# Optimization experiments

Hardware: AMD Instinct MI355X
Metric: run time of the kernel (lower is better)

Reference implementation:

```python
import jax, jax.numpy as jnp
import numpy as np

B, IN, H, NOPT = 16384, 4096, 128, 64
GAIN = 0.5  # default control_gains value in the module


def gru_cell(x, h, Wih, Whh, bih, bhh):
    # torch GRU single step; gate order r, z, n
    gi = x @ Wih + bih          # [B, 3H]
    gh = h @ Whh + bhh          # [B, 3H]
    ir, iz, inn = jnp.split(gi, 3, axis=-1)
    hr, hz, hn = jnp.split(gh, 3, axis=-1)
    r = jax.nn.sigmoid(ir + hr)
    z = jax.nn.sigmoid(iz + hz)
    n = jnp.tanh(inn + r * hn)
    return (1.0 - z) * n + z * h


def setup_inputs() -> dict:
    key = jax.random.key(0)
    ks = jax.random.split(key, 12)
    s = lambda k, shape: (jax.random.normal(k, shape, jnp.float32) * 0.05)
    return {
        "obs": jax.random.normal(ks[0], (B, IN), jnp.float32),
        "chosen_option": jax.random.randint(ks[1], (B,), 0, NOPT),
        "h0": jnp.zeros((B, H), jnp.float32),
        "h1": jnp.zeros((B, H), jnp.float32),
        "Wa": s(ks[2], (IN, H)), "ba": jnp.zeros((H,), jnp.float32),
        "Wih0": s(ks[3], (H, 3 * H)), "Whh0": s(ks[4], (H, 3 * H)),
        "bih0": jnp.zeros((3 * H,), jnp.float32), "bhh0": jnp.zeros((3 * H,), jnp.float32),
        "Wih1": s(ks[5], (2 * H, 3 * H)), "Whh1": s(ks[6], (H, 3 * H)),
        "bih1": jnp.zeros((3 * H,), jnp.float32), "bhh1": jnp.zeros((3 * H,), jnp.float32),
        "Wv0": s(ks[7], (H, NOPT)), "bv0": jnp.zeros((NOPT,), jnp.float32),
        "Wv1": s(ks[8], (H, NOPT)), "bv1": jnp.zeros((NOPT,), jnp.float32),
        "Wt0": s(ks[9], (H, NOPT)), "bt0": jnp.zeros((NOPT,), jnp.float32),
    }


def reference(obs, chosen_option, h0, h1, Wa, ba, Wih0, Whh0, bih0, bhh0,
              Wih1, Whh1, bih1, bhh1, Wv0, bv0, Wv1, bv1, Wt0, bt0):
    # attention: tanh(Linear(obs))
    attn = jnp.tanh(obs @ Wa + ba)                       # [B, H]
    # layer 0: GRU on attn
    h0n = gru_cell(attn, h0, Wih0, Whh0, bih0, bhh0)     # [B, H]
    hc0 = (h0n - 0.5) * GAIN + 0.5                       # gain contrast
    v0 = hc0 @ Wv0 + bv0                                 # [B, NOPT]
    term = jax.nn.sigmoid(hc0 @ Wt0 + bt0)               # [B, NOPT]
    term_p = jnp.take_along_axis(term, chosen_option[:, None], axis=1)  # [B, 1]
    # layer 1: GRU on cat(attn, own hidden)
    x1 = jnp.concatenate([attn, h1], axis=-1)            # [B, 2H]
    h1n = gru_cell(x1, h1, Wih1, Whh1, bih1, bhh1)       # [B, H]
    hc1 = (h1n - 0.5) * GAIN + 0.5
    v1 = hc1 @ Wv1 + bv1                                 # [B, NOPT]
    return v0, term_p, v1, h0n, h1n
```

## Files before the change

kernel.cpp:

```cpp
#include <hip/hip_runtime.h>
#include <stdint.h>


typedef __attribute__((ext_vector_type(8))) short bf16x8;
typedef __attribute__((ext_vector_type(4))) float f32x4;
typedef __attribute__((ext_vector_type(8))) float f32x8;

#define INDIM 4096
#define H 128
#define NOPT 64

#define WS_WAT    0u
#define WS_WIH0T  524288u
#define WS_WHH0T  573440u
#define WS_WIH1T  622592u
#define WS_WHH1T  720896u
#define WS_WV0T   770048u
#define WS_WV1T   778240u
#define WS_WT0T   786432u

#define OUT_V0    0u
#define OUT_TERMP 1048576u
#define OUT_V1    1064960u
#define OUT_H0N   2113536u
#define OUT_H1N   4210688u

static __device__ __forceinline__ uint16_t f2bf(float f) {
  union { float f; uint32_t i; } x; x.f = f;
  uint32_t r = x.i + 0x7fffu + ((x.i >> 16) & 1u);
  return (uint16_t)(r >> 16);
}
static __device__ __forceinline__ float sigm(float x) { return 1.0f / (1.0f + __expf(-x)); }
static __device__ __forceinline__ float fast_tanh(float x) {
  float e = __expf(2.0f * x);
  return 1.0f - 2.0f / (e + 1.0f);
}
static __device__ __forceinline__ f32x4 mfma16(bf16x8 a, bf16x8 b, f32x4 c) {
  return __builtin_amdgcn_mfma_f32_16x16x32_bf16(a, b, c, 0, 0, 0);
}
static __device__ __forceinline__ bf16x8 cvt8(f32x8 v) {
  bf16x8 r;
#pragma unroll
  for (int j = 0; j < 8; ++j) r[j] = (short)f2bf(v[j]);
  return r;
}

__global__ void k_transpose(const float* __restrict__ Wa,
                            const float* __restrict__ Wih0,
                            const float* __restrict__ Whh0,
                            const float* __restrict__ Wih1,
                            const float* __restrict__ Whh1,
                            const float* __restrict__ Wv0,
                            const float* __restrict__ Wv1,
                            const float* __restrict__ Wt0,
                            uint16_t* __restrict__ ws) {
  int blk = blockIdx.x;
  const float* in; uint16_t* out; int ksh; int N; int base;
  if (blk < 2048)      { in = Wa;   out = ws + WS_WAT;   ksh = 12; N = 128; base = 0; }
  else if (blk < 2240) { in = Wih0; out = ws + WS_WIH0T; ksh = 7;  N = 384; base = 2048; }
  else if (blk < 2432) { in = Whh0; out = ws + WS_WHH0T; ksh = 7;  N = 384; base = 2240; }
  else if (blk < 2816) { in = Wih1; out = ws + WS_WIH1T; ksh = 8;  N = 384; base = 2432; }
  else if (blk < 3008) { in = Whh1; out = ws + WS_WHH1T; ksh = 7;  N = 384; base = 2816; }
  else if (blk < 3040) { in = Wv0;  out = ws + WS_WV0T;  ksh = 7;  N = 64;  base = 3008; }
  else if (blk < 3072) { in = Wv1;  out = ws + WS_WV1T;  ksh = 7;  N = 64;  base = 3040; }
  else                 { in = Wt0;  out = ws + WS_WT0T;  ksh = 7;  N = 64;  base = 3072; }
  int e = (blk - base) * 256 + (int)threadIdx.x;
  int n = e >> ksh;
  int k = e & ((1 << ksh) - 1);
  out[e] = f2bf(in[(size_t)k * N + n]);
}

__launch_bounds__(128)
__global__ void k_fused(const float* __restrict__ obs,
                        const uint16_t* __restrict__ ws,
                        const float* __restrict__ ba,
                        const float* __restrict__ h0,
                        const float* __restrict__ bih0,
                        const float* __restrict__ bhh0,
                        const float* __restrict__ bv0,
                        const float* __restrict__ bt0,
                        const int* __restrict__ chosen,
                        const float* __restrict__ h1,
                        const float* __restrict__ bih1,
                        const float* __restrict__ bhh1,
                        const float* __restrict__ bv1,
                        float* __restrict__ out) {
  __shared__ uint16_t sAttn[2][16 * 16 * 8];
  __shared__ uint16_t sHC[2][16 * 16 * 8];
  const uint16_t* WaT   = ws + WS_WAT;
  const uint16_t* Wih0T = ws + WS_WIH0T;
  const uint16_t* Whh0T = ws + WS_WHH0T;
  const uint16_t* Wih1T = ws + WS_WIH1T;
  const uint16_t* Whh1T = ws + WS_WHH1T;
  const uint16_t* Wv0T  = ws + WS_WV0T;
  const uint16_t* Wv1T  = ws + WS_WV1T;
  const uint16_t* Wt0T  = ws + WS_WT0T;
  const int t = threadIdx.x, w = t >> 6, lane = t & 63;
  const int l15 = lane & 15, quad = lane >> 4;
  const int row0 = blockIdx.x * 32 + w * 16;
  uint16_t* sX = sAttn[w];
  uint16_t* sC = sHC[w];

  f32x4 acc[8] = {};
  {
    const float* arow = obs + (size_t)(row0 + l15) * INDIM + quad * 8;
    const uint16_t* brow = WaT + (size_t)l15 * INDIM + quad * 8;
#pragma unroll 2
    for (int kt = 0; kt < 64; ++kt) {
      const int k0 = kt * 64;
      f32x8 av0 = *(const f32x8*)(arow + k0);
      f32x8 av1 = *(const f32x8*)(arow + k0 + 32);
      bf16x8 a0 = cvt8(av0);
      bf16x8 a1 = cvt8(av1);
#pragma unroll
      for (int nb = 0; nb < 8; ++nb) {
        const uint16_t* bp = brow + (size_t)(nb * 16) * INDIM + k0;
        bf16x8 b0 = *(const bf16x8*)(bp);
        bf16x8 b1 = *(const bf16x8*)(bp + 32);
        acc[nb] = mfma16(a0, b0, acc[nb]);
        acc[nb] = mfma16(a1, b1, acc[nb]);
      }
    }
  }
#pragma unroll
  for (int nb = 0; nb < 8; ++nb) {
    const int col = nb * 16 + l15;
    const float bav = ba[col];
    const int kb = col >> 3;
#pragma unroll
    for (int i = 0; i < 4; ++i) {
      const int r = quad * 4 + i;
      sX[(r * 16 + (kb ^ r)) * 8 + (col & 7)] = f2bf(fast_tanh(acc[nb][i] + bav));
    }
  }

  bf16x8 ax[4], ah[4];
  {
    const float* hrow = h0 + (size_t)(row0 + l15) * H + quad * 8;
#pragma unroll
    for (int ks = 0; ks < 4; ++ks) {
      const int kb = ks * 4 + quad;
      ax[ks] = *(const bf16x8*)&sX[(l15 * 16 + (kb ^ l15)) * 8];
      ah[ks] = cvt8(*(const f32x8*)(hrow + ks * 32));
    }
  }
#pragma unroll
  for (int nb = 0; nb < 8; ++nb) {
    f32x4 air = {}, ahr = {}, aiz = {}, ahz = {}, ain = {}, ahn = {};
    const int nrow = nb * 16 + l15;
#pragma unroll
    for (int ks = 0; ks < 4; ++ks) {
      const int k = ks * 32 + quad * 8;
      bf16x8 b;
      b = *(const bf16x8*)(Wih0T + (size_t)(nrow      ) * H + k); air = mfma16(ax[ks], b, air);
      b = *(const bf16x8*)(Wih0T + (size_t)(nrow + 128) * H + k); aiz = mfma16(ax[ks], b, aiz);
      b = *(const bf16x8*)(Wih0T + (size_t)(nrow + 256) * H + k); ain = mfma16(ax[ks], b, ain);
      b = *(const bf16x8*)(Whh0T + (size_t)(nrow      ) * H + k); ahr = mfma16(ah[ks], b, ahr);
      b = *(const bf16x8*)(Whh0T + (size_t)(nrow + 128) * H + k); ahz = mfma16(ah[ks], b, ahz);
      b = *(const bf16x8*)(Whh0T + (size_t)(nrow + 256) * H + k); ahn = mfma16(ah[ks], b, ahn);
    }
    const int col = nrow;
    const float b_ir = bih0[col],       b_hr = bhh0[col];
    const float b_iz = bih0[col + 128], b_hz = bhh0[col + 128];
    const float b_in = bih0[col + 256], b_hn = bhh0[col + 256];
    const int kb = col >> 3;
#pragma unroll
    for (int i = 0; i < 4; ++i) {
      const int r = quad * 4 + i;
      const int grow = row0 + r;
      const float rr = sigm(air[i] + ahr[i] + b_ir + b_hr);
      const float zz = sigm(aiz[i] + ahz[i] + b_iz + b_hz);
      const float nn = fast_tanh(ain[i] + b_in + rr * (ahn[i] + b_hn));
      const float hv = h0[(size_t)grow * H + col];
      const float hnew = (1.0f - zz) * nn + zz * hv;
      out[OUT_H0N + (size_t)grow * H + col] = hnew;
      sC[(r * 16 + (kb ^ r)) * 8 + (col & 7)] = f2bf(0.5f * hnew + 0.25f);
    }
  }
  {
    int ch[4];
#pragma unroll
    for (int i = 0; i < 4; ++i) ch[i] = chosen[row0 + quad * 4 + i];
    bf16x8 ac[4];
#pragma unroll
    for (int ks = 0; ks < 4; ++ks) {
      const int kb = ks * 4 + quad;
      ac[ks] = *(const bf16x8*)&sC[(l15 * 16 + (kb ^ l15)) * 8];
    }
#pragma unroll
    for (int vb = 0; vb < 4; ++vb) {
      f32x4 av = {}, at = {};
      const int nrow = vb * 16 + l15;
#pragma unroll
      for (int ks = 0; ks < 4; ++ks) {
        const int k = ks * 32 + quad * 8;
        bf16x8 b;
        b = *(const bf16x8*)(Wv0T + (size_t)nrow * H + k); av = mfma16(ac[ks], b, av);
        b = *(const bf16x8*)(Wt0T + (size_t)nrow * H + k); at = mfma16(ac[ks], b, at);
      }
      const int col = vb * 16 + l15;
      const float bvv = bv0[col], btv = bt0[col];
#pragma unroll
      for (int i = 0; i < 4; ++i) {
        const int grow = row0 + quad * 4 + i;
        out[OUT_V0 + (size_t)grow * NOPT + col] = av[i] + bvv;
        if (ch[i] == col)
          out[OUT_TERMP + grow] = sigm(at[i] + btv);
      }
    }
  }

  bf16x8 ah1[4];
  {
    const float* hrow = h1 + (size_t)(row0 + l15) * H + quad * 8;
#pragma unroll
    for (int ks = 0; ks < 4; ++ks)
      ah1[ks] = cvt8(*(const f32x8*)(hrow + ks * 32));
  }
#pragma unroll
  for (int nb = 0; nb < 8; ++nb) {
    f32x4 air = {}, ahr = {}, aiz = {}, ahz = {}, ain = {}, ahn = {};
    const int nrow = nb * 16 + l15;
#pragma unroll
    for (int ks = 0; ks < 8; ++ks) {
      const int k = ks * 32 + quad * 8;
      const bf16x8 a = (ks < 4) ? ax[ks] : ah1[ks - 4];
      bf16x8 b;
      b = *(const bf16x8*)(Wih1T + (size_t)(nrow      ) * 256 + k); air = mfma16(a, b, air);
      b = *(const bf16x8*)(Wih1T + (size_t)(nrow + 128) * 256 + k); aiz = mfma16(a, b, aiz);
      b = *(const bf16x8*)(Wih1T + (size_t)(nrow + 256) * 256 + k); ain = mfma16(a, b, ain);
    }
#pragma unroll
    for (int ks = 0; ks < 4; ++ks) {
      const int k = ks * 32 + quad * 8;
      bf16x8 b;
      b = *(const bf16x8*)(Whh1T + (size_t)(nrow      ) * H + k); ahr = mfma16(ah1[ks], b, ahr);
      b = *(const bf16x8*)(Whh1T + (size_t)(nrow + 128) * H + k); ahz = mfma16(ah1[ks], b, ahz);
      b = *(const bf16x8*)(Whh1T + (size_t)(nrow + 256) * H + k); ahn = mfma16(ah1[ks], b, ahn);
    }
    const int col = nrow;
    const float b_ir = bih1[col],       b_hr = bhh1[col];
    const float b_iz = bih1[col + 128], b_hz = bhh1[col + 128];
    const float b_in = bih1[col + 256], b_hn = bhh1[col + 256];
    const int kb = col >> 3;
#pragma unroll
    for (int i = 0; i < 4; ++i) {
      const int r = quad * 4 + i;
      const int grow = row0 + r;
      const float rr = sigm(air[i] + ahr[i] + b_ir + b_hr);
      const float zz = sigm(aiz[i] + ahz[i] + b_iz + b_hz);
      const float nn = fast_tanh(ain[i] + b_in + rr * (ahn[i] + b_hn));
      const float hv = h1[(size_t)grow * H + col];
      const float hnew = (1.0f - zz) * nn + zz * hv;
      out[OUT_H1N + (size_t)grow * H + col] = hnew;
      sC[(r * 16 + (kb ^ r)) * 8 + (col & 7)] = f2bf(0.5f * hnew + 0.25f);
    }
  }
  {
    bf16x8 ac[4];
#pragma unroll
    for (int ks = 0; ks < 4; ++ks) {
      const int kb = ks * 4 + quad;
      ac[ks] = *(const bf16x8*)&sC[(l15 * 16 + (kb ^ l15)) * 8];
    }
#pragma unroll
    for (int vb = 0; vb < 4; ++vb) {
      f32x4 av = {};
      const int nrow = vb * 16 + l15;
#pragma unroll
      for (int ks = 0; ks < 4; ++ks) {
        const int k = ks * 32 + quad * 8;
        bf16x8 b = *(const bf16x8*)(Wv1T + (size_t)nrow * H + k);
        av = mfma16(ac[ks], b, av);
      }
      const int col = vb * 16 + l15;
      const float bvv = bv1[col];
#pragma unroll
      for (int i = 0; i < 4; ++i) {
        const int grow = row0 + quad * 4 + i;
        out[OUT_V1 + (size_t)grow * NOPT + col] = av[i] + bvv;
      }
    }
  }
}

extern "C" void kernel_launch(void* const* d_in, const int* in_sizes, int n_in,
                              void* d_out, int out_size, void* d_ws, size_t ws_size,
                              hipStream_t stream) {
  (void)in_sizes; (void)n_in; (void)out_size; (void)ws_size;
  const float* obs    = (const float*)d_in[0];
  const int*   chosen = (const int*)d_in[1];
  const float* h0     = (const float*)d_in[2];
  const float* h1     = (const float*)d_in[3];
  const float* Wa     = (const float*)d_in[4];
  const float* ba     = (const float*)d_in[5];
  const float* Wih0   = (const float*)d_in[6];
  const float* Whh0   = (const float*)d_in[7];
  const float* bih0   = (const float*)d_in[8];
  const float* bhh0   = (const float*)d_in[9];
  const float* Wih1   = (const float*)d_in[10];
  const float* Whh1   = (const float*)d_in[11];
  const float* bih1   = (const float*)d_in[12];
  const float* bhh1   = (const float*)d_in[13];
  const float* Wv0    = (const float*)d_in[14];
  const float* bv0    = (const float*)d_in[15];
  const float* Wv1    = (const float*)d_in[16];
  const float* bv1    = (const float*)d_in[17];
  const float* Wt0    = (const float*)d_in[18];
  const float* bt0    = (const float*)d_in[19];
  uint16_t* ws  = (uint16_t*)d_ws;
  float*    out = (float*)d_out;

  hipLaunchKernelGGL(k_transpose, dim3(3104), dim3(256), 0, stream,
                     Wa, Wih0, Whh0, Wih1, Whh1, Wv0, Wv1, Wt0, ws);
  hipLaunchKernelGGL(k_fused, dim3(512), dim3(128), 0, stream,
                     obs, ws, ba, h0, bih0, bhh0, bv0, bt0, chosen,
                     h1, bih1, bhh1, bv1, out);
}
```

Baseline: 539.3 us.

## Split GRU columns across four waves per 16-row block to raise occupancy

Each block now handles 16 batch rows with 4 waves, and each wave computes 32 of the 128 hidden columns. The attention GEMM, both GRU cells and the value heads are partitioned the same way, with shared-memory tiles and __syncthreads between stages. The grid grows from 512×128 to 1024×256 threads, so many more waves are in flight to hide load latency on the large obs stream. The cost is that every wave re-reads and re-converts the same obs rows, relying on cache hits, and the kernel now needs block-wide barriers. The float-to-bf16 conversion also switches to the HIP intrinsic, which may map to a hardware instruction.

```diff
diff --git a/kernel.cpp b/kernel.cpp
--- a/kernel.cpp
+++ b/kernel.cpp
@@ -1,4 +1,5 @@
 #include <hip/hip_runtime.h>
+#include <hip/hip_bf16.h>
 #include <stdint.h>
 
 
@@ -26,9 +27,8 @@
 #define OUT_H1N   4210688u
 
 static __device__ __forceinline__ uint16_t f2bf(float f) {
-  union { float f; uint32_t i; } x; x.f = f;
-  uint32_t r = x.i + 0x7fffu + ((x.i >> 16) & 1u);
-  return (uint16_t)(r >> 16);
+  __hip_bfloat16 h = __float2bfloat16(f);
+  return __builtin_bit_cast(uint16_t, h);
 }
 static __device__ __forceinline__ float sigm(float x) { return 1.0f / (1.0f + __expf(-x)); }
 static __device__ __forceinline__ float fast_tanh(float x) {
@@ -70,7 +70,7 @@
   out[e] = f2bf(in[(size_t)k * N + n]);
 }
 
-__launch_bounds__(128)
+__launch_bounds__(256, 4)
 __global__ void k_fused(const float* __restrict__ obs,
                         const uint16_t* __restrict__ ws,
                         const float* __restrict__ ba,
@@ -85,8 +85,8 @@
                         const float* __restrict__ bhh1,
                         const float* __restrict__ bv1,
                         float* __restrict__ out) {
-  __shared__ uint16_t sAttn[2][16 * 16 * 8];
-  __shared__ uint16_t sHC[2][16 * 16 * 8];
+  __shared__ uint16_t sX[16 * 16 * 8];
+  __shared__ uint16_t sC[16 * 16 * 8];
   const uint16_t* WaT   = ws + WS_WAT;
   const uint16_t* Wih0T = ws + WS_WIH0T;
   const uint16_t* Whh0T = ws + WS_WHH0T;
@@ -97,42 +97,44 @@
   const uint16_t* Wt0T  = ws + WS_WT0T;
   const int t = threadIdx.x, w = t >> 6, lane = t & 63;
   const int l15 = lane & 15, quad = lane >> 4;
-  const int row0 = blockIdx.x * 32 + w * 16;
-  uint16_t* sX = sAttn[w];
-  uint16_t* sC = sHC[w];
-
-  f32x4 acc[8] = {};
-  {
-    const float* arow = obs + (size_t)(row0 + l15) * INDIM + quad * 8;
-    const uint16_t* brow = WaT + (size_t)l15 * INDIM + quad * 8;
+  const int row0 = blockIdx.x * 16;
+  const int nbA = 2 * w;
+
+  f32x4 acc0 = {}, acc1 = {};
+  {
+    const float*    arow  = obs + (size_t)(row0 + l15) * INDIM + quad * 8;
+    const uint16_t* brow0 = WaT + (size_t)(nbA * 16 + l15) * INDIM + quad * 8;
+    const uint16_t* brow1 = brow0 + (size_t)16 * INDIM;
 #pragma unroll 2
     for (int kt = 0; kt < 64; ++kt) {
       const int k0 = kt * 64;
       f32x8 av0 = *(const f32x8*)(arow + k0);
       f32x8 av1 = *(const f32x8*)(arow + k0 + 32);
+      bf16x8 b00 = *(const bf16x8*)(brow0 + k0);
+      bf16x8 b01 = *(const bf16x8*)(brow0 + k0 + 32);
+      bf16x8 b10 = *(const bf16x8*)(brow1 + k0);
+      bf16x8 b11 = *(const bf16x8*)(brow1 + k0 + 32);
       bf16x8 a0 = cvt8(av0);
       bf16x8 a1 = cvt8(av1);
-#pragma unroll
-      for (int nb = 0; nb < 8; ++nb) {
-        const uint16_t* bp = brow + (size_t)(nb * 16) * INDIM + k0;
-        bf16x8 b0 = *(const bf16x8*)(bp);
-        bf16x8 b1 = *(const bf16x8*)(bp + 32);
-        acc[nb] = mfma16(a0, b0, acc[nb]);
-        acc[nb] = mfma16(a1, b1, acc[nb]);
-      }
-    }
-  }
-#pragma unroll
-  for (int nb = 0; nb < 8; ++nb) {
-    const int col = nb * 16 + l15;
+      acc0 = mfma16(a0, b00, acc0);
+      acc0 = mfma16(a1, b01, acc0);
+      acc1 = mfma16(a0, b10, acc1);
+      acc1 = mfma16(a1, b11, acc1);
+    }
+  }
+#pragma unroll
+  for (int nbl = 0; nbl < 2; ++nbl) {
+    const f32x4 A = nbl ? acc1 : acc0;
+    const int col = (nbA + nbl) * 16 + l15;
     const float bav = ba[col];
     const int kb = col >> 3;
 #pragma unroll
     for (int i = 0; i < 4; ++i) {
       const int r = quad * 4 + i;
-      sX[(r * 16 + (kb ^ r)) * 8 + (col & 7)] = f2bf(fast_tanh(acc[nb][i] + bav));
-    }
-  }
+      sX[(r * 16 + (kb ^ r)) * 8 + (col & 7)] = f2bf(fast_tanh(A[i] + bav));
+    }
+  }
+  __syncthreads();
 
   bf16x8 ax[4], ah[4];
   {
@@ -145,9 +147,9 @@
     }
   }
 #pragma unroll
-  for (int nb = 0; nb < 8; ++nb) {
+  for (int nbl = 0; nbl < 2; ++nbl) {
+    const int nrow = (nbA + nbl) * 16 + l15;
     f32x4 air = {}, ahr = {}, aiz = {}, ahz = {}, ain = {}, ahn = {};
-    const int nrow = nb * 16 + l15;
 #pragma unroll
     for (int ks = 0; ks < 4; ++ks) {
       const int k = ks * 32 + quad * 8;
@@ -177,6 +179,8 @@
       sC[(r * 16 + (kb ^ r)) * 8 + (col & 7)] = f2bf(0.5f * hnew + 0.25f);
     }
   }
+  __syncthreads();
+
   {
     int ch[4];
 #pragma unroll
@@ -187,28 +191,26 @@
       const int kb = ks * 4 + quad;
       ac[ks] = *(const bf16x8*)&sC[(l15 * 16 + (kb ^ l15)) * 8];
     }
-#pragma unroll
-    for (int vb = 0; vb < 4; ++vb) {
-      f32x4 av = {}, at = {};
-      const int nrow = vb * 16 + l15;
-#pragma unroll
-      for (int ks = 0; ks < 4; ++ks) {
-        const int k = ks * 32 + quad * 8;
-        bf16x8 b;
-        b = *(const bf16x8*)(Wv0T + (size_t)nrow * H + k); av = mfma16(ac[ks], b, av);
-        b = *(const bf16x8*)(Wt0T + (size_t)nrow * H + k); at = mfma16(ac[ks], b, at);
-      }
-      const int col = vb * 16 + l15;
-      const float bvv = bv0[col], btv = bt0[col];
-#pragma unroll
-      for (int i = 0; i < 4; ++i) {
-        const int grow = row0 + quad * 4 + i;
-        out[OUT_V0 + (size_t)grow * NOPT + col] = av[i] + bvv;
-        if (ch[i] == col)
-          out[OUT_TERMP + grow] = sigm(at[i] + btv);
-      }
-    }
-  }
+    f32x4 av = {}, at = {};
+    const int nrow = w * 16 + l15;
+#pragma unroll
+    for (int ks = 0; ks < 4; ++ks) {
+      const int k = ks * 32 + quad * 8;
+      bf16x8 b;
+      b = *(const bf16x8*)(Wv0T + (size_t)nrow * H + k); av = mfma16(ac[ks], b, av);
+      b = *(const bf16x8*)(Wt0T + (size_t)nrow * H + k); at = mfma16(ac[ks], b, at);
+    }
+    const int col = nrow;
+    const float bvv = bv0[col], btv = bt0[col];
+#pragma unroll
+    for (int i = 0; i < 4; ++i) {
+      const int grow = row0 + quad * 4 + i;
+      out[OUT_V0 + (size_t)grow * NOPT + col] = av[i] + bvv;
+      if (ch[i] == col)
+        out[OUT_TERMP + grow] = sigm(at[i] + btv);
+    }
+  }
+  __syncthreads();
 
   bf16x8 ah1[4];
   {
@@ -218,9 +220,9 @@
       ah1[ks] = cvt8(*(const f32x8*)(hrow + ks * 32));
   }
 #pragma unroll
-  for (int nb = 0; nb < 8; ++nb) {
+  for (int nbl = 0; nbl < 2; ++nbl) {
+    const int nrow = (nbA + nbl) * 16 + l15;
     f32x4 air = {}, ahr = {}, aiz = {}, ahz = {}, ain = {}, ahn = {};
-    const int nrow = nb * 16 + l15;
 #pragma unroll
     for (int ks = 0; ks < 8; ++ks) {
       const int k = ks * 32 + quad * 8;
@@ -256,6 +258,8 @@
       sC[(r * 16 + (kb ^ r)) * 8 + (col & 7)] = f2bf(0.5f * hnew + 0.25f);
     }
   }
+  __syncthreads();
+
   {
     bf16x8 ac[4];
 #pragma unroll
@@ -263,23 +267,20 @@
       const int kb = ks * 4 + quad;
       ac[ks] = *(const bf16x8*)&sC[(l15 * 16 + (kb ^ l15)) * 8];
     }
-#pragma unroll
-    for (int vb = 0; vb < 4; ++vb) {
-      f32x4 av = {};
-      const int nrow = vb * 16 + l15;
-#pragma unroll
-      for (int ks = 0; ks < 4; ++ks) {
-        const int k = ks * 32 + quad * 8;
-        bf16x8 b = *(const bf16x8*)(Wv1T + (size_t)nrow * H + k);
-        av = mfma16(ac[ks], b, av);
-      }
-      const int col = vb * 16 + l15;
-      const float bvv = bv1[col];
-#pragma unroll
-      for (int i = 0; i < 4; ++i) {
-        const int grow = row0 + quad * 4 + i;
-        out[OUT_V1 + (size_t)grow * NOPT + col] = av[i] + bvv;
-      }
+    f32x4 av = {};
+    const int nrow = w * 16 + l15;
+#pragma unroll
+    for (int ks = 0; ks < 4; ++ks) {
+      const int k = ks * 32 + quad * 8;
+      bf16x8 b = *(const bf16x8*)(Wv1T + (size_t)nrow * H + k);
+      av = mfma16(ac[ks], b, av);
+    }
+    const int col = nrow;
+    const float bvv = bv1[col];
+#pragma unroll
+    for (int i = 0; i < 4; ++i) {
+      const int grow = row0 + quad * 4 + i;
+      out[OUT_V1 + (size_t)grow * NOPT + col] = av[i] + bvv;
     }
   }
 }
@@ -313,7 +314,7 @@
 
   hipLaunchKernelGGL(k_transpose, dim3(3104), dim3(256), 0, stream,
                      Wa, Wih0, Whh0, Wih1, Whh1, Wv0, Wv1, Wt0, ws);
-  hipLaunchKernelGGL(k_fused, dim3(512), dim3(128), 0, stream,
+  hipLaunchKernelGGL(k_fused, dim3(1024), dim3(256), 0, stream,
                      obs, ws, ba, h0, bih0, bhh0, bv0, bt0, chosen,
                      h1, bih1, bhh1, bv1, out);
 }
```

Result: slower. 620.5 us (+15.1%).
